# Performance work log

Measured on AMD Instinct MI355X. Metric: run time of the kernel, lower is better.

## Reference

```python
import jax, jax.numpy as jnp
import numpy as np

D_MODEL = 2048
NUM_HEADS = 16
HEAD_DIM = D_MODEL // NUM_HEADS


def _rotary(x, head_dim):
    # x: (..., T, head_dim). Matches torch module: half-split rotation.
    T = x.shape[-2]
    pos = jnp.arange(T, dtype=jnp.float32)[:, None]              # (T,1)
    dim = jnp.arange(head_dim // 2, dtype=jnp.float32)[None, :]  # (1,hd/2)
    angle = pos * (1.0 / jnp.power(10000.0, 2.0 * dim / head_dim))
    cos = jnp.cos(angle)  # (T, hd/2), broadcasts over leading dims
    sin = jnp.sin(angle)
    x1 = x[..., : head_dim // 2]
    x2 = x[..., head_dim // 2:]
    return jnp.concatenate([x1 * cos - x2 * sin, x2 * cos + x1 * sin], axis=-1)


def setup_inputs() -> dict:
    key = jax.random.key(0)
    ks = jax.random.split(key, 9)
    B, T, D, H, HD = 2, 2048, D_MODEL, NUM_HEADS, HEAD_DIM
    s = 1.0 / np.sqrt(D)
    return {
        "x": jax.random.normal(ks[0], (B, T, D), jnp.float32),
        "Wq": jax.random.normal(ks[1], (D, D), jnp.float32) * s,
        "bq": jnp.zeros((D,), jnp.float32),
        "Wk": jax.random.normal(ks[2], (D, HD), jnp.float32) * s,
        "bk": jnp.zeros((HD,), jnp.float32),
        "Wv": jax.random.normal(ks[3], (D, HD), jnp.float32) * s,
        "bv": jnp.zeros((HD,), jnp.float32),
        "Wo": jax.random.normal(ks[4], (D, D), jnp.float32) * s,
        "bo": jnp.zeros((D,), jnp.float32),
    }


def reference(x, Wq, bq, Wk, bk, Wv, bv, Wo, bo):
    B, T, D = x.shape
    H, HD = NUM_HEADS, HEAD_DIM
    q = (x @ Wq + bq).reshape(B, T, H, HD).transpose(0, 2, 1, 3)  # (B,H,T,hd)
    k = (x @ Wk + bk)[:, None]                                    # (B,1,T,hd)
    v = (x @ Wv + bv)[:, None]                                    # (B,1,T,hd)
    q = _rotary(q, HD)
    k = _rotary(k, HD)
    scores = jnp.einsum("bhqd,bhkd->bhqk", q, jnp.broadcast_to(k, (B, 1, T, HD))) / jnp.sqrt(jnp.float32(HD))
    attn = jax.nn.softmax(scores, axis=-1)                        # (B,H,T,T)
    ctx = jnp.einsum("bhqk,bhkd->bhqd", attn, jnp.broadcast_to(v, (B, 1, T, HD)))
    ctx = ctx.transpose(0, 2, 1, 3).reshape(B, T, D)
    return ctx @ Wo + bo
```

## Files before the change

### kernel.cpp

```cpp
#include <hip/hip_runtime.h>
#include <math.h>

#define T_SEQ  2048
#define DMODEL 2048
#define NHEADS 16
#define HDIM   128
#define MROWS  4096

typedef __attribute__((ext_vector_type(8)))  __bf16 bf16x8;
typedef __attribute__((ext_vector_type(4)))  __bf16 bf16x4;
typedef __attribute__((ext_vector_type(4)))  float  f32x4;
typedef __attribute__((ext_vector_type(16))) float  f32x16;
typedef __attribute__((ext_vector_type(4)))  unsigned int uint32x4;

#define GLOBAL_AS __attribute__((address_space(1)))
#define LDS_AS    __attribute__((address_space(3)))
__device__ __forceinline__ void async_copy16(const __bf16* g, __bf16* l) {
  __builtin_amdgcn_global_load_lds((const GLOBAL_AS void*)g, (LDS_AS void*)l, 16, 0, 0);
}

__device__ __forceinline__ unsigned int pack_bf16_2(float a, float b) {
  __bf16 x = (__bf16)a, y = (__bf16)b;
  unsigned short ux = __builtin_bit_cast(unsigned short, x);
  unsigned short uy = __builtin_bit_cast(unsigned short, y);
  return (unsigned int)ux | ((unsigned int)uy << 16);
}

__global__ __launch_bounds__(256) void prep_kernel(
    const float* __restrict__ x,
    const float* __restrict__ Wq, const float* __restrict__ Wk,
    const float* __restrict__ Wv, const float* __restrict__ Wo,
    float2* __restrict__ rope, __bf16* __restrict__ xb,
    __bf16* __restrict__ wqkvt, __bf16* __restrict__ wot)
{
  __shared__ float t[32][33];
  const int bid = blockIdx.x;
  const int tid = threadIdx.x;

  if (bid < 512) {
    int idx = bid*256 + tid;
    int d = idx & 63, pos = idx >> 6;
    double freq = pow(10000.0, -(double)d / 64.0);
    double ang = (double)pos * freq;
    rope[idx] = make_float2((float)cos(ang), (float)sin(ang));
    return;
  }
  if (bid < 512 + 8192) {
    int i = (bid - 512)*256 + tid;
    float4 v = ((const float4*)x)[i];
    bf16x4 o = { (__bf16)v.x, (__bf16)v.y, (__bf16)v.z, (__bf16)v.w };
    *(bf16x4*)(xb + (size_t)i*4) = o;
    return;
  }
  const int lb = bid - (512 + 8192);
  const int by = lb / 136;
  const int bx = lb - by*136;
  const float* src; __bf16* dst; int istride, c0, orow;
  if (bx < 64)       { src = Wq; istride = 2048; c0 = bx*32;      orow = c0;        dst = wqkvt; }
  else if (bx < 68)  { src = Wk; istride = 128;  c0 = (bx-64)*32; orow = 2048 + c0; dst = wqkvt; }
  else if (bx < 72)  { src = Wv; istride = 128;  c0 = (bx-68)*32; orow = 2176 + c0; dst = wqkvt; }
  else               { src = Wo; istride = 2048; c0 = (bx-72)*32; orow = c0;        dst = wot; }
  const int tx = tid & 31, ty = tid >> 5;
  const int r0 = by*32;
#pragma unroll
  for (int i = 0; i < 4; ++i)
    t[ty + i*8][tx] = src[(size_t)(r0 + ty + i*8)*istride + c0 + tx];
  __syncthreads();
#pragma unroll
  for (int i = 0; i < 4; ++i)
    dst[(size_t)(orow + ty + i*8)*2048 + r0 + tx] = (__bf16)t[tx][ty + i*8];
}

__global__ void transpose_v_kernel(const __bf16* __restrict__ in,
                                   __bf16* __restrict__ out) {
  __shared__ __bf16 t[32][34];
  const int bz = blockIdx.z;
  in  += (size_t)bz * 2048 * 128;
  out += (size_t)bz * 128 * 2048;
  const int tx = threadIdx.x & 31, ty = threadIdx.x >> 5;
  const int r0 = blockIdx.y*32, c0 = blockIdx.x*32;
#pragma unroll
  for (int i = 0; i < 4; ++i)
    t[ty + i*8][tx] = in[(size_t)(r0 + ty + i*8)*128 + c0 + tx];
  __syncthreads();
#pragma unroll
  for (int i = 0; i < 4; ++i)
    out[(size_t)(c0 + ty + i*8)*2048 + r0 + tx] = t[tx][ty + i*8];
}

__global__ __launch_bounds__(256) void gemm_qkv_fused(
    const __bf16* __restrict__ A,
    const __bf16* __restrict__ Bt,
    const float* __restrict__ bq, const float* __restrict__ bk,
    const float* __restrict__ bv,
    const float2* __restrict__ rope,
    __bf16* __restrict__ qrb,
    __bf16* __restrict__ kbb,
    __bf16* __restrict__ vbb,
    float qscale)
{
  __shared__ __bf16 As[128*32];
  __shared__ __bf16 Bs[128*32];
  const int tid = threadIdx.x;
  const int lane = tid & 63, wave = tid >> 6;
  const int quad = lane >> 4, l16 = lane & 15;
  const int m0 = (wave >> 1)*64, n0 = (wave & 1)*32;
  const int row0 = blockIdx.y*128, col0 = blockIdx.x*128;
  const int srow = lane >> 2, scol = (lane & 3)*8;

  f32x4 acc[4][4];
#pragma unroll
  for (int i = 0; i < 4; ++i)
#pragma unroll
    for (int j = 0; j < 4; ++j) acc[i][j] = (f32x4){0.f,0.f,0.f,0.f};

  const __bf16* Ag = A  + (size_t)(row0 + wave*32 + srow)*DMODEL + scol;
  const __bf16* Bg = Bt + (size_t)(col0 + wave*32 + srow)*DMODEL + scol;
  __bf16* AsW = &As[wave*1024];
  __bf16* BsW = &Bs[wave*1024];

  for (int kk = 0; kk < DMODEL; kk += 32) {
    __syncthreads();
    async_copy16(Ag + kk,                     AsW);
    async_copy16(Ag + kk + (size_t)16*DMODEL, AsW + 512);
    async_copy16(Bg + kk,                     BsW);
    async_copy16(Bg + kk + (size_t)16*DMODEL, BsW + 512);
    __syncthreads();
    bf16x8 af[4], bfr[4];
#pragma unroll
    for (int i = 0; i < 4; ++i)
      af[i] = *(const bf16x8*)&As[(m0 + i*16 + l16)*32 + quad*8];
#pragma unroll
    for (int j = 0; j < 4; ++j) {
      const int cb = n0 + (j & 1)*16 + (j >> 1)*64;
      bfr[j] = *(const bf16x8*)&Bs[(cb + l16)*32 + quad*8];
    }
#pragma unroll
    for (int i = 0; i < 4; ++i)
#pragma unroll
      for (int j = 0; j < 4; ++j)
        acc[i][j] = __builtin_amdgcn_mfma_f32_16x16x32_bf16(af[i], bfr[j], acc[i][j], 0,0,0);
  }

  const int bx = blockIdx.x;
  const float* bias_p; float scale; bool rot; __bf16* obase; int ostride;
  if (bx < 16)      { bias_p = bq + bx*128; scale = qscale; rot = true;
                      obase = qrb + bx*128; ostride = 2048; }
  else if (bx == 16){ bias_p = bk; scale = 1.f; rot = true;
                      obase = kbb; ostride = 128; }
  else              { bias_p = bv; scale = 1.f; rot = false;
                      obase = vbb; ostride = 128; }

#pragma unroll
  for (int j = 0; j < 2; ++j) {
    const int d = n0 + j*16 + l16;
    const float b1 = bias_p[d], b2 = bias_p[d + 64];
#pragma unroll
    for (int i = 0; i < 4; ++i) {
      const int rl = m0 + i*16 + quad*4;
#pragma unroll
      for (int r = 0; r < 4; ++r) {
        const int rg = row0 + rl + r;
        const float x1 = acc[i][j][r]   + b1;
        const float x2 = acc[i][j+2][r] + b2;
        float c = 1.f, s = 0.f;
        if (rot) { float2 cs = rope[(size_t)(rg & (T_SEQ-1))*64 + d]; c = cs.x; s = cs.y; }
        obase[(size_t)rg*ostride + d]      = (__bf16)((x1*c - x2*s)*scale);
        obase[(size_t)rg*ostride + d + 64] = (__bf16)((x2*c + x1*s)*scale);
      }
    }
  }
}

__global__ __launch_bounds__(256) void gemm_bf16_t128(
    const __bf16* __restrict__ A, const __bf16* __restrict__ Bt,
    const float* __restrict__ bias, float* __restrict__ C,
    int M, int N, int K)
{
  __shared__ __bf16 As[128*32];
  __shared__ __bf16 Bs[128*32];
  const int tid = threadIdx.x;
  const int lane = tid & 63, wave = tid >> 6;
  const int quad = lane >> 4, l16 = lane & 15;
  const int m0 = (wave & 1)*64, n0 = (wave >> 1)*64;
  const int row0 = blockIdx.y*128, col0 = blockIdx.x*128;
  const int srow = lane >> 2, scol = (lane & 3)*8;

  f32x4 acc[4][4];
#pragma unroll
  for (int i = 0; i < 4; ++i)
#pragma unroll
    for (int j = 0; j < 4; ++j) acc[i][j] = (f32x4){0.f,0.f,0.f,0.f};

  const __bf16* Ag = A  + (size_t)(row0 + wave*32 + srow)*K + scol;
  const __bf16* Bg = Bt + (size_t)(col0 + wave*32 + srow)*K + scol;
  __bf16* AsW = &As[wave*1024];
  __bf16* BsW = &Bs[wave*1024];

  for (int kk = 0; kk < K; kk += 32) {
    __syncthreads();
    async_copy16(Ag + kk,              AsW);
    async_copy16(Ag + kk + (size_t)16*K, AsW + 512);
    async_copy16(Bg + kk,              BsW);
    async_copy16(Bg + kk + (size_t)16*K, BsW + 512);
    __syncthreads();
    bf16x8 af[4], bfr[4];
#pragma unroll
    for (int i = 0; i < 4; ++i)
      af[i] = *(const bf16x8*)&As[(m0 + i*16 + l16)*32 + quad*8];
#pragma unroll
    for (int j = 0; j < 4; ++j)
      bfr[j] = *(const bf16x8*)&Bs[(n0 + j*16 + l16)*32 + quad*8];
#pragma unroll
    for (int i = 0; i < 4; ++i)
#pragma unroll
      for (int j = 0; j < 4; ++j)
        acc[i][j] = __builtin_amdgcn_mfma_f32_16x16x32_bf16(af[i], bfr[j], acc[i][j], 0,0,0);
  }
#pragma unroll
  for (int j = 0; j < 4; ++j) {
    const int ccol = col0 + n0 + j*16 + l16;
    const float bvv = bias[ccol];
#pragma unroll
    for (int i = 0; i < 4; ++i) {
      const int crow = row0 + m0 + i*16 + quad*4;
#pragma unroll
      for (int r = 0; r < 4; ++r)
        C[(size_t)(crow + r)*N + ccol] = acc[i][j][r] + bvv;
    }
  }
}

#define KSTR 136
#define VSTR 72
__global__ __launch_bounds__(256) void mqa_attn_mfma(
    const __bf16* __restrict__ qb,
    const __bf16* __restrict__ kb,
    const __bf16* __restrict__ vt,
    __bf16* __restrict__ ctx)
{
  __shared__ __bf16 Ks[64*KSTR];
  __shared__ __bf16 Vs[128*VSTR];
  __shared__ float  Linv[128];
  const int tid = threadIdx.x, lane = tid & 63, wave = tid >> 6;
  const int h5 = lane >> 5, l32 = lane & 31;
  const int h = blockIdx.y, b = blockIdx.z;
  const int qbase = blockIdx.x*128 + wave*32;

  bf16x8 qf[8];
  const __bf16* qp = qb + ((size_t)b*T_SEQ + qbase + l32)*DMODEL + h*HDIM;
#pragma unroll
  for (int ds = 0; ds < 8; ++ds) qf[ds] = *(const bf16x8*)(qp + ds*16 + h5*8);

  f32x16 oacc[4];
#pragma unroll
  for (int g = 0; g < 4; ++g)
#pragma unroll
    for (int r = 0; r < 16; ++r) oacc[g][r] = 0.f;
  float lsum = 0.f;

  const __bf16* kbase = kb + (size_t)b*T_SEQ*HDIM;
  const __bf16* vbase = vt + (size_t)b*HDIM*T_SEQ;

  for (int kt = 0; kt < T_SEQ/64; ++kt) {
    __syncthreads();
#pragma unroll
    for (int i = 0; i < 4; ++i) {
      int idx = i*256 + tid;
      int key = idx >> 4, c = idx & 15;
      *(bf16x8*)&Ks[key*KSTR + c*8] =
          *(const bf16x8*)(kbase + (size_t)(kt*64 + key)*HDIM + c*8);
    }
#pragma unroll
    for (int i = 0; i < 4; ++i) {
      int idx = i*256 + tid;
      int d = idx >> 3, c = idx & 7;
      *(bf16x8*)&Vs[d*VSTR + c*8] =
          *(const bf16x8*)(vbase + (size_t)d*T_SEQ + kt*64 + c*8);
    }
    __syncthreads();

    f32x16 sacc[2];
#pragma unroll
    for (int kg = 0; kg < 2; ++kg) {
#pragma unroll
      for (int r = 0; r < 16; ++r) sacc[kg][r] = 0.f;
      __builtin_amdgcn_s_setprio(1);
#pragma unroll
      for (int ds = 0; ds < 8; ++ds) {
        bf16x8 kf = *(const bf16x8*)&Ks[(kg*32 + l32)*KSTR + ds*16 + h5*8];
        sacc[kg] = __builtin_amdgcn_mfma_f32_32x32x16_bf16(kf, qf[ds], sacc[kg], 0,0,0);
      }
      __builtin_amdgcn_s_setprio(0);
    }

    bf16x8 pf[4];
#pragma unroll
    for (int kg = 0; kg < 2; ++kg) {
      unsigned int w[8];
#pragma unroll
      for (int m = 0; m < 8; ++m) {
        float p0 = __builtin_amdgcn_exp2f(sacc[kg][2*m]);
        float p1 = __builtin_amdgcn_exp2f(sacc[kg][2*m+1]);
        lsum += p0; lsum += p1;
        w[m] = pack_bf16_2(p0, p1);
      }
#pragma unroll
      for (int kss = 0; kss < 2; ++kss) {
        auto s1 = __builtin_amdgcn_permlane32_swap(w[4*kss+0], w[4*kss+2], false, false);
        auto s2 = __builtin_amdgcn_permlane32_swap(w[4*kss+1], w[4*kss+3], false, false);
        uint32x4 u = (uint32x4){ s1[0], s2[0], s1[1], s2[1] };
        pf[kg*2 + kss] = __builtin_bit_cast(bf16x8, u);
      }
    }

    __builtin_amdgcn_s_setprio(1);
#pragma unroll
    for (int ks = 0; ks < 4; ++ks) {
#pragma unroll
      for (int g = 0; g < 4; ++g) {
        bf16x8 vf = *(const bf16x8*)&Vs[(g*32 + l32)*VSTR + ks*16 + h5*8];
        oacc[g] = __builtin_amdgcn_mfma_f32_32x32x16_bf16(pf[ks], vf, oacc[g], 0,0,0);
      }
    }
    __builtin_amdgcn_s_setprio(0);
  }

  lsum += __shfl_xor(lsum, 32);
  if (h5 == 0) Linv[wave*32 + l32] = 1.f / lsum;
  __asm__ volatile("s_waitcnt lgkmcnt(0)" ::: "memory");

  __bf16* op = ctx + ((size_t)b*T_SEQ + qbase)*DMODEL + h*HDIM + l32;
#pragma unroll
  for (int r1 = 0; r1 < 4; ++r1) {
    float4 iv = *(const float4*)&Linv[wave*32 + r1*8 + h5*4];
#pragma unroll
    for (int r0 = 0; r0 < 4; ++r0) {
      int qrow = r1*8 + h5*4 + r0;
#pragma unroll
      for (int g = 0; g < 4; ++g)
        op[(size_t)qrow*DMODEL + g*32] = (__bf16)(oacc[g][r1*4 + r0] * (&iv.x)[r0]);
    }
  }
}

extern "C" void kernel_launch(void* const* d_in, const int* in_sizes, int n_in,
                              void* d_out, int out_size, void* d_ws, size_t ws_size,
                              hipStream_t stream) {
  const float* x  = (const float*)d_in[0];
  const float* Wq = (const float*)d_in[1];
  const float* bq = (const float*)d_in[2];
  const float* Wk = (const float*)d_in[3];
  const float* bk = (const float*)d_in[4];
  const float* Wv = (const float*)d_in[5];
  const float* bv = (const float*)d_in[6];
  const float* Wo = (const float*)d_in[7];
  const float* bo = (const float*)d_in[8];
  float* out = (float*)d_out;

  uint8_t* ws = (uint8_t*)d_ws;
  __bf16* qrb  = (__bf16*)(ws);
  __bf16* xb   = (__bf16*)(ws + 16777216);
  __bf16* wqkvt= (__bf16*)(ws + 33554432);
  __bf16* wot  = (__bf16*)(ws + 42991616);
  __bf16* kbb  = (__bf16*)(ws + 51380224);
  __bf16* vbb  = (__bf16*)(ws + 52428800);
  __bf16* vtb  = (__bf16*)(ws + 53477376);
  float2* rope = (float2*)(ws + 54525952);

  const float qscale = 1.4426950408889634f * 0.08838834764831845f;

  prep_kernel<<<dim3(17408), 256, 0, stream>>>(x, Wq, Wk, Wv, Wo, rope, xb, wqkvt, wot);

  gemm_qkv_fused<<<dim3(18,32), 256, 0, stream>>>(
      xb, wqkvt, bq, bk, bv, rope, qrb, kbb, vbb, qscale);

  transpose_v_kernel<<<dim3(4,64,2), 256, 0, stream>>>(vbb, vtb);

  mqa_attn_mfma<<<dim3(16,16,2), 256, 0, stream>>>(qrb, kbb, vtb, xb);

  gemm_bf16_t128<<<dim3(16,32), 256, 0, stream>>>(xb, wot, bo, out, MROWS, DMODEL, DMODEL);
}
```

Before: 312.4 us.

## Fuse V transpose into QKV GEMM epilogue and remap GEMM blocks across XCDs

The QKV GEMM epilogue now writes V directly in transposed layout with bf16x4 vector stores, which removes the separate transpose kernel launch and its round trip through memory. The rotary branch becomes unconditional for the Q/K blocks. Both GEMMs switch to a 1D grid with a block-index remap, (id&7)*q + (id>>3), so consecutive workgroups on each of the 8 XCDs share tiles and get better L2 reuse. The remap assumes the grid size is divisible by 8.

```diff
diff --git a/kernel.cpp b/kernel.cpp
--- a/kernel.cpp
+++ b/kernel.cpp
@@ -71,23 +71,6 @@
     dst[(size_t)(orow + ty + i*8)*2048 + r0 + tx] = (__bf16)t[tx][ty + i*8];
 }
 
-__global__ void transpose_v_kernel(const __bf16* __restrict__ in,
-                                   __bf16* __restrict__ out) {
-  __shared__ __bf16 t[32][34];
-  const int bz = blockIdx.z;
-  in  += (size_t)bz * 2048 * 128;
-  out += (size_t)bz * 128 * 2048;
-  const int tx = threadIdx.x & 31, ty = threadIdx.x >> 5;
-  const int r0 = blockIdx.y*32, c0 = blockIdx.x*32;
-#pragma unroll
-  for (int i = 0; i < 4; ++i)
-    t[ty + i*8][tx] = in[(size_t)(r0 + ty + i*8)*128 + c0 + tx];
-  __syncthreads();
-#pragma unroll
-  for (int i = 0; i < 4; ++i)
-    out[(size_t)(c0 + ty + i*8)*2048 + r0 + tx] = t[tx][ty + i*8];
-}
-
 __global__ __launch_bounds__(256) void gemm_qkv_fused(
     const __bf16* __restrict__ A,
     const __bf16* __restrict__ Bt,
@@ -96,16 +79,19 @@
     const float2* __restrict__ rope,
     __bf16* __restrict__ qrb,
     __bf16* __restrict__ kbb,
-    __bf16* __restrict__ vbb,
+    __bf16* __restrict__ vtb,
     float qscale)
 {
   __shared__ __bf16 As[128*32];
   __shared__ __bf16 Bs[128*32];
+  const int orig = blockIdx.x;
+  const int wgid = (orig & 7)*72 + (orig >> 3);
+  const int by = wgid & 31, bx = wgid >> 5;
   const int tid = threadIdx.x;
   const int lane = tid & 63, wave = tid >> 6;
   const int quad = lane >> 4, l16 = lane & 15;
   const int m0 = (wave >> 1)*64, n0 = (wave & 1)*32;
-  const int row0 = blockIdx.y*128, col0 = blockIdx.x*128;
+  const int row0 = by*128, col0 = bx*128;
   const int srow = lane >> 2, scol = (lane & 3)*8;
 
   f32x4 acc[4][4];
@@ -142,14 +128,33 @@
         acc[i][j] = __builtin_amdgcn_mfma_f32_16x16x32_bf16(af[i], bfr[j], acc[i][j], 0,0,0);
   }
 
-  const int bx = blockIdx.x;
-  const float* bias_p; float scale; bool rot; __bf16* obase; int ostride;
-  if (bx < 16)      { bias_p = bq + bx*128; scale = qscale; rot = true;
+  if (bx == 17) {
+#pragma unroll
+    for (int j = 0; j < 2; ++j) {
+      const int d = n0 + j*16 + l16;
+      const float b1 = bv[d], b2 = bv[d + 64];
+#pragma unroll
+      for (int i = 0; i < 4; ++i) {
+        const int rg = row0 + m0 + i*16 + quad*4;
+        const int bb = rg >> 11, t0 = rg & (T_SEQ-1);
+        bf16x4 p1, p2;
+#pragma unroll
+        for (int r = 0; r < 4; ++r) {
+          p1[r] = (__bf16)(acc[i][j][r]   + b1);
+          p2[r] = (__bf16)(acc[i][j+2][r] + b2);
+        }
+        *(bf16x4*)&vtb[((size_t)bb*128 + d)*T_SEQ + t0]      = p1;
+        *(bf16x4*)&vtb[((size_t)bb*128 + d + 64)*T_SEQ + t0] = p2;
+      }
+    }
+    return;
+  }
+
+  const float* bias_p; float scale; __bf16* obase; int ostride;
+  if (bx < 16)      { bias_p = bq + bx*128; scale = qscale;
                       obase = qrb + bx*128; ostride = 2048; }
-  else if (bx == 16){ bias_p = bk; scale = 1.f; rot = true;
+  else              { bias_p = bk; scale = 1.f;
                       obase = kbb; ostride = 128; }
-  else              { bias_p = bv; scale = 1.f; rot = false;
-                      obase = vbb; ostride = 128; }
 
 #pragma unroll
   for (int j = 0; j < 2; ++j) {
@@ -163,10 +168,9 @@
         const int rg = row0 + rl + r;
         const float x1 = acc[i][j][r]   + b1;
         const float x2 = acc[i][j+2][r] + b2;
-        float c = 1.f, s = 0.f;
-        if (rot) { float2 cs = rope[(size_t)(rg & (T_SEQ-1))*64 + d]; c = cs.x; s = cs.y; }
-        obase[(size_t)rg*ostride + d]      = (__bf16)((x1*c - x2*s)*scale);
-        obase[(size_t)rg*ostride + d + 64] = (__bf16)((x2*c + x1*s)*scale);
+        float2 cs = rope[(size_t)(rg & (T_SEQ-1))*64 + d];
+        obase[(size_t)rg*ostride + d]      = (__bf16)((x1*cs.x - x2*cs.y)*scale);
+        obase[(size_t)rg*ostride + d + 64] = (__bf16)((x2*cs.x + x1*cs.y)*scale);
       }
     }
   }
@@ -179,11 +183,17 @@
 {
   __shared__ __bf16 As[128*32];
   __shared__ __bf16 Bs[128*32];
+  const int nwg = gridDim.x;
+  const int rowTiles = M >> 7;
+  const int q = nwg >> 3;
+  const int orig = blockIdx.x;
+  const int wgid = (orig & 7)*q + (orig >> 3);
+  const int by = wgid % rowTiles, bx = wgid / rowTiles;
   const int tid = threadIdx.x;
   const int lane = tid & 63, wave = tid >> 6;
   const int quad = lane >> 4, l16 = lane & 15;
   const int m0 = (wave & 1)*64, n0 = (wave >> 1)*64;
-  const int row0 = blockIdx.y*128, col0 = blockIdx.x*128;
+  const int row0 = by*128, col0 = bx*128;
   const int srow = lane >> 2, scol = (lane & 3)*8;
 
   f32x4 acc[4][4];
@@ -364,7 +374,6 @@
   __bf16* wqkvt= (__bf16*)(ws + 33554432);
   __bf16* wot  = (__bf16*)(ws + 42991616);
   __bf16* kbb  = (__bf16*)(ws + 51380224);
-  __bf16* vbb  = (__bf16*)(ws + 52428800);
   __bf16* vtb  = (__bf16*)(ws + 53477376);
   float2* rope = (float2*)(ws + 54525952);
 
@@ -372,12 +381,10 @@
 
   prep_kernel<<<dim3(17408), 256, 0, stream>>>(x, Wq, Wk, Wv, Wo, rope, xb, wqkvt, wot);
 
-  gemm_qkv_fused<<<dim3(18,32), 256, 0, stream>>>(
-      xb, wqkvt, bq, bk, bv, rope, qrb, kbb, vbb, qscale);
-
-  transpose_v_kernel<<<dim3(4,64,2), 256, 0, stream>>>(vbb, vtb);
+  gemm_qkv_fused<<<dim3(576), 256, 0, stream>>>(
+      xb, wqkvt, bq, bk, bv, rope, qrb, kbb, vtb, qscale);
 
   mqa_attn_mfma<<<dim3(16,16,2), 256, 0, stream>>>(qrb, kbb, vtb, xb);
 
-  gemm_bf16_t128<<<dim3(16,32), 256, 0, stream>>>(xb, wot, bo, out, MROWS, DMODEL, DMODEL);
-}
+  gemm_bf16_t128<<<dim3(512), 256, 0, stream>>>(xb, wot, bo, out, MROWS, DMODEL, DMODEL);
+}
```

After: 335.7 us. 1.07x slower.
